# Optimization experiments

Measured on AMD Instinct MI355X. Metric: run time of the kernel, lower is better.

The kernel has to match this reference:

```python
import jax, jax.numpy as jnp
import numpy as np

NUM_TAGS = 5

def setup_inputs() -> dict:
    key = jax.random.key(0)
    ks = jax.random.split(key, 8)
    B, N, K, Q = 2, 5, 5, 4
    Ls, Lq, D = 128, 128, 768
    inp = {
        'support_token_embedding': jax.random.normal(ks[0], (B * N * K, Ls, D), jnp.float32),
        'query_token_embedding': jax.random.normal(ks[1], (B * N * Q, Lq, D), jnp.float32),
        'support_mask': jnp.ones((B * N * K, Ls), jnp.float32),
        'query_mask': jnp.ones((B * N * Q, Lq), jnp.float32),
        'support_entity_label': jax.random.normal(ks[2], (B * N * K, Ls, NUM_TAGS), jnp.float32),
        'proj_w': jax.random.normal(ks[3], (D, 4 * D), jnp.float32) * 0.02,
        'proj_b': jnp.zeros((D,), jnp.float32),
        'rel_w1': jax.random.normal(ks[4], (D, 4 * D), jnp.float32) * 0.02,
        'rel_b1': jnp.zeros((D,), jnp.float32),
        'rel_w2': jax.random.normal(ks[5], (1, D), jnp.float32) * 0.02,
        'rel_b2': jnp.zeros((1,), jnp.float32),
        'B': B, 'N': N, 'K': K, 'Q': Q,
    }
    return inp

def _fuse(m1, m2):
    return jnp.concatenate([m1, m2, jnp.abs(m1 - m2), m1 * m2], axis=-1)

def reference(support_token_embedding, query_token_embedding, support_mask, query_mask,
              support_entity_label, proj_w, proj_b, rel_w1, rel_b1, rel_w2, rel_b2,
              B, N, K, Q):
    D = support_token_embedding.shape[-1]
    Lq = query_token_embedding.shape[1]

    # ---- cal_bio: per-(sample,shot) tag prototypes, vectorized ----
    labels = jnp.argmax(support_entity_label, axis=-1)                 # [BNK, Ls]
    onehot = jax.nn.one_hot(labels, NUM_TAGS, dtype=jnp.float32)       # [BNK, Ls, T]
    # tag 0 ('O') is additionally gated by the support mask
    masks = jnp.concatenate([onehot[:, :, :1] * support_mask[:, :, None], onehot[:, :, 1:]], axis=2)
    sums = jnp.einsum('blt,bld->btd', masks, support_token_embedding)  # [BNK, T, D]
    cnt = jnp.sum(masks, axis=1)[:, :, None]                           # [BNK, T, 1]
    proto = jnp.where(cnt > 0, sums / jnp.maximum(cnt, 1.0), 0.0)      # [BNK, T, D]
    proto = proto.reshape(B * N, K, NUM_TAGS, D).mean(axis=1)          # mean over K shots
    proto = proto.reshape(B, N, NUM_TAGS, D)                           # support_BIO

    # ---- expand to all (query, class) pairs: batch = B*N*Q*N ----
    BQ = B * N * Q * N
    support = jnp.broadcast_to(proto[:, None], (B, N * Q, N, NUM_TAGS, D)).reshape(BQ, NUM_TAGS, D)
    query = jnp.broadcast_to(query_token_embedding.reshape(B, N * Q, 1, Lq, D),
                             (B, N * Q, N, Lq, D)).reshape(BQ, Lq, D)
    qmask = jnp.broadcast_to(query_mask.reshape(B, N * Q, 1, Lq),
                             (B, N * Q, N, Lq)).reshape(BQ, Lq, 1)
    smask = jnp.ones((BQ, NUM_TAGS, 1), jnp.float32)

    # ---- CoAttention with additive mask bias + post-softmax mask multiply ----
    att = jnp.einsum('bsd,bqd->bsq', support, query) + smask * jnp.swapaxes(qmask, 1, 2) * 100.0
    support_ = jnp.einsum('bsq,bqd->bsd', jax.nn.softmax(att, axis=2), query) * smask
    query_ = jnp.einsum('bqs,bsd->bqd', jax.nn.softmax(jnp.swapaxes(att, 1, 2), axis=2), support) * qmask

    # ---- fuse + proj + relu ----
    es = jax.nn.relu(_fuse(support, support_) @ proj_w.T + proj_b)     # [BQ, T, D]
    eq = jax.nn.relu(_fuse(query, query_) @ proj_w.T + proj_b)        # [BQ, Lq, D]

    # ---- local aggregation: masked max + mean pooling ----
    eq_agg = jnp.concatenate([jnp.max(eq, axis=1), jnp.sum(eq, axis=1) / jnp.sum(qmask, axis=1)], axis=1)
    es_agg = jnp.concatenate([jnp.max(es, axis=1), jnp.sum(es, axis=1) / jnp.sum(smask, axis=1)], axis=1)

    # ---- relation MLP ----
    cat_seq = jnp.concatenate([eq_agg, es_agg], axis=1)                # [BQ, 4D]
    h = jax.nn.relu(cat_seq @ rel_w1.T + rel_b1)
    logits = h @ rel_w2.T + rel_b2                                     # [BQ, 1]
    return logits.reshape(B * N * Q, N)
```

## Files before the change

### kernel.cpp

```cpp
#include <hip/hip_runtime.h>

typedef unsigned short u16;
typedef __attribute__((ext_vector_type(8))) short short8;
typedef __attribute__((ext_vector_type(4))) float f32x4;

#define B_   2
#define N_   5
#define K_   5
#define Q_   4
#define T_   5
#define D_   768
#define L_   128
#define BN_  (B_*N_)
#define BNK_ (B_*N_*K_)
#define BQ_  (B_*N_*Q_*N_)
#define K4_  (4*D_)
#define KFQ  1536
#define AROWS 144

#define QEMB_N  (40*128*768)
#define PROJW_N (768*3072)
#define R_PROTO1 5120
#define R_SUP    5248
#define R_PROTO2 6248
#define R_TOTAL  6400

__device__ __forceinline__ float bf2f(u16 u) {
    return __uint_as_float(((unsigned)u) << 16);
}
__device__ __forceinline__ u16 f2bf(float f) {
    unsigned u = __float_as_uint(f);
    return (u16)((u + 0x7fffu + ((u >> 16) & 1u)) >> 16);
}
__device__ __forceinline__ void gl_lds16(const u16* g, u16* l) {
    __builtin_amdgcn_global_load_lds(
        (const __attribute__((address_space(1))) unsigned int*)g,
        (__attribute__((address_space(3))) unsigned int*)l, 16, 0, 0);
}

__global__ void k_convert3(const float* __restrict__ q, const float* __restrict__ pw,
                           const float* __restrict__ rw, u16* __restrict__ qo,
                           u16* __restrict__ po, u16* __restrict__ ro) {
    const long n1 = QEMB_N / 4, n2 = PROJW_N / 4;
    const long total = n1 + 2 * n2;
    for (long i = (long)blockIdx.x * 256 + threadIdx.x; i < total; i += (long)gridDim.x * 256) {
        const float* src; u16* dst; long k;
        if (i < n1)            { src = q;  dst = qo; k = i; }
        else if (i < n1 + n2)  { src = pw; dst = po; k = i - n1; }
        else                   { src = rw; dst = ro; k = i - n1 - n2; }
        float4 v = ((const float4*)src)[k];
        u16 o[4] = {f2bf(v.x), f2bf(v.y), f2bf(v.z), f2bf(v.w)};
        *(uint2*)(dst + k * 4) = *(const uint2*)o;
    }
}

__global__ void k_proto_shot(const float* __restrict__ label, const float* __restrict__ smask,
                             const float* __restrict__ semb, float* __restrict__ proto_shot) {
    int bnk = blockIdx.x;
    int s = blockIdx.y;
    __shared__ int   s_tag[L_];
    __shared__ float s_w[L_];
    __shared__ float s_cnt[T_];
    int tid = threadIdx.x;
    if (tid < L_) {
        const float* lp = label + ((long)bnk * L_ + tid) * T_;
        float best = lp[0]; int bi = 0;
        #pragma unroll
        for (int t = 1; t < T_; ++t) { float v = lp[t]; if (v > best) { best = v; bi = t; } }
        s_tag[tid] = bi;
        s_w[tid]   = (bi == 0) ? smask[(long)bnk * L_ + tid] : 1.0f;
    }
    __syncthreads();
    if (tid < T_) {
        float c = 0.f;
        for (int l = 0; l < L_; ++l) if (s_tag[l] == tid) c += s_w[l];
        s_cnt[tid] = c;
    }
    __syncthreads();
    float acc[T_] = {};
    for (int l = 0; l < L_; ++l) {
        float w = s_w[l]; int tg = s_tag[l];
        float e = semb[((long)bnk * L_ + l) * D_ + tid + s * 256] * w;
        #pragma unroll
        for (int t = 0; t < T_; ++t) acc[t] += (tg == t) ? e : 0.0f;
    }
    int d = tid + s * 256;
    #pragma unroll
    for (int t = 0; t < T_; ++t) {
        float c = s_cnt[t];
        float v = (c > 0.f) ? acc[t] / fmaxf(c, 1.f) : 0.f;
        proto_shot[(bnk * T_ + t) * D_ + d] = v;
    }
}

__global__ void k_proto_mean(const float* __restrict__ proto_shot,
                             float* __restrict__ proto_f32, u16* __restrict__ A_all) {
    int bx = blockIdx.x;
    if (bx < 150) {
        int idx = bx * 256 + threadIdx.x;
        if (idx >= BN_ * T_ * D_) return;
        int r = idx / D_, d = idx - r * D_;
        int bn = r / T_;
        int rem = idx - bn * (T_ * D_);
        float s = 0.f;
        #pragma unroll
        for (int k = 0; k < K_; ++k) s += proto_shot[(bn * K_ + k) * (T_ * D_) + rem];
        s *= (1.f / K_);
        proto_f32[idx] = s;
        u16 b = f2bf(s);
        A_all[(size_t)(R_PROTO1 + r) * D_ + d] = b;
        A_all[(size_t)(R_PROTO2 + r) * D_ + d] = b;
    } else {
        int zidx = (bx - 150) * 256 + threadIdx.x;
        if (zidx >= 59904 + 78336) return;
        size_t off;
        if (zidx < 59904) off = (size_t)5170 * D_ + zidx;
        else              off = (size_t)6298 * D_ + (zidx - 59904);
        A_all[off] = 0;
    }
}

__global__ void k_attn(const float* __restrict__ qemb, const float* __restrict__ qmask_g,
                       const float* __restrict__ proto_f32,
                       u16* __restrict__ qf, u16* __restrict__ supA,
                       float* __restrict__ p2m_ws, float* __restrict__ qssum_ws) {
    int x = blockIdx.x;
    int xcd = x & 7, slot = x >> 3;
    int g = (slot / 5) * 8 + xcd;
    int n2 = slot % 5;
    int bq = g * 5 + n2;
    int q_idx = g;
    int bn = (bq / (N_ * Q_ * N_)) * N_ + (bq % N_);
    __shared__ float s_proto[T_ * D_];
    __shared__ float s_att[T_][L_];
    __shared__ float s_ps[T_][L_];
    __shared__ float s_qm[L_];
    int tid = threadIdx.x;
    for (int i = tid; i < T_ * D_; i += 256) s_proto[i] = proto_f32[bn * T_ * D_ + i];
    if (tid < L_) s_qm[tid] = qmask_g[(long)q_idx * L_ + tid];
    __syncthreads();
    for (int p = tid; p < T_ * L_; p += 256) {
        int t = p >> 7, q = p & (L_ - 1);
        const float* pp = s_proto + t * D_;
        const float4* qp = (const float4*)(qemb + ((size_t)q_idx * L_ + q) * D_);
        float acc = 0.f;
        #pragma unroll 4
        for (int d = 0; d < D_ / 4; ++d) {
            float4 v = qp[d];
            acc += v.x * pp[4 * d] + v.y * pp[4 * d + 1] + v.z * pp[4 * d + 2] + v.w * pp[4 * d + 3];
        }
        s_att[t][q] = acc + 100.f * s_qm[q];
    }
    __syncthreads();
    if (tid < T_) {
        int t = tid; float m = -1e30f;
        for (int q = 0; q < L_; ++q) m = fmaxf(m, s_att[t][q]);
        float ss = 0.f;
        for (int q = 0; q < L_; ++q) { float e = __expf(s_att[t][q] - m); s_ps[t][q] = e; ss += e; }
        float inv = 1.f / ss;
        for (int q = 0; q < L_; ++q) s_ps[t][q] *= inv;
    } else if (tid >= 128) {
        int q = tid - 128; float m = -1e30f;
        float e[T_];
        #pragma unroll
        for (int t = 0; t < T_; ++t) m = fmaxf(m, s_att[t][q]);
        float ss = 0.f;
        #pragma unroll
        for (int t = 0; t < T_; ++t) { e[t] = __expf(s_att[t][q] - m); ss += e[t]; }
        float inv = s_qm[q] / ss;
        #pragma unroll
        for (int t = 0; t < T_; ++t) p2m_ws[((size_t)bq * T_ + t) * L_ + q] = e[t] * inv;
    } else if (tid == 5) {
        float s = 0.f;
        for (int q = 0; q < L_; ++q) s += s_qm[q];
        qssum_ws[bq] = s;
    }
    __syncthreads();
    u16* qfb = qf + (size_t)bq * AROWS * KFQ;
    {
        float acc[T_][3] = {};
        #pragma unroll 4
        for (int q = 0; q < L_; ++q) {
            const float* qp = qemb + ((size_t)q_idx * L_ + q) * D_;
            float qv[3];
            #pragma unroll
            for (int s = 0; s < 3; ++s) qv[s] = qp[tid + s * 256];
            #pragma unroll
            for (int t = 0; t < T_; ++t) {
                float p = s_ps[t][q];
                #pragma unroll
                for (int s = 0; s < 3; ++s) acc[t][s] += p * qv[s];
            }
        }
        #pragma unroll
        for (int t = 0; t < T_; ++t) {
            u16* er = qfb + (size_t)(128 + t) * KFQ;
            #pragma unroll
            for (int s = 0; s < 3; ++s) {
                int d = tid + s * 256;
                float p = s_proto[t * D_ + d];
                float sv = acc[t][s];
                supA[((size_t)bq * T_ + t) * D_ + d] = f2bf(sv);
                er[d]       = f2bf(fabsf(p - sv));
                er[768 + d] = f2bf(p * sv);
            }
        }
    }
    {
        u16* pr2 = qfb + (size_t)133 * KFQ;
        short8 z = short8{0, 0, 0, 0, 0, 0, 0, 0};
        for (int i = tid; i < (11 * KFQ) / 8; i += 256) *(short8*)(pr2 + i * 8) = z;
    }
}

__global__ void k_qf(const float* __restrict__ qemb, const float* __restrict__ proto_f32,
                     const float* __restrict__ p2m, u16* __restrict__ qf) {
    int bq = blockIdx.x;
    int rg = blockIdx.y;
    int q_idx = bq / N_;
    int bn = (bq / (N_ * Q_ * N_)) * N_ + (bq % N_);
    __shared__ float s_proto[T_ * D_];
    __shared__ float s_p2[32][8];
    int tid = threadIdx.x;
    int w = tid >> 6, lane = tid & 63;
    for (int i = tid; i < T_ * D_; i += 256) s_proto[i] = proto_f32[bn * T_ * D_ + i];
    if (tid < 32 * T_) {
        int r = tid / T_, t = tid - r * T_;
        s_p2[r][t] = p2m[((size_t)bq * T_ + t) * L_ + rg * 32 + r];
    }
    __syncthreads();
    u16* qfb = qf + (size_t)bq * AROWS * KFQ;
    #pragma unroll
    for (int rr = 0; rr < 8; ++rr) {
        int rloc = w * 8 + rr;
        int row = rg * 32 + rloc;
        float p0 = s_p2[rloc][0], p1 = s_p2[rloc][1], p2v = s_p2[rloc][2];
        float p3 = s_p2[rloc][3], p4 = s_p2[rloc][4];
        const float* qrow = qemb + ((size_t)q_idx * L_ + row) * D_;
        u16* qr = qfb + (size_t)row * KFQ;
        #pragma unroll
        for (int ch = 0; ch < 12; ++ch) {
            int c = ch * 64 + lane;
            float m2 = p0 * s_proto[c] + p1 * s_proto[D_ + c] + p2v * s_proto[2 * D_ + c]
                     + p3 * s_proto[3 * D_ + c] + p4 * s_proto[4 * D_ + c];
            float qv = qrow[c];
            qr[c]       = f2bf(fabsf(qv - m2));
            qr[768 + c] = f2bf(qv * m2);
        }
    }
}

#define SUBGW ((128 + 128) * 32)
__global__ __launch_bounds__(256) void k_gemm_gw(const u16* __restrict__ A_all,
                                                 const u16* __restrict__ projw_bf,
                                                 u16* __restrict__ g1, u16* __restrict__ sw2,
                                                 u16* __restrict__ pw2) {
    int mbase = blockIdx.y * 128;
    int jbase = blockIdx.x * 128;
    int boff = (mbase >= R_SUP) ? 768 : 0;
    __shared__ __align__(16) u16 sT[2][2 * SUBGW];
    int tid = threadIdx.x;
    int lane = tid & 63, w = tid >> 6, quad = lane >> 4, l16 = lane & 15;
    int srow = lane >> 2, sko = lane & 3;
    const u16* Ab = A_all + ((size_t)mbase + srow) * D_ + sko * 8;
    const u16* Bb = projw_bf + (size_t)(jbase + srow) * K4_ + boff + sko * 8;

    f32x4 zero = {0.f, 0.f, 0.f, 0.f};
    f32x4 acc[8][2];
    #pragma unroll
    for (int rt = 0; rt < 8; ++rt) { acc[rt][0] = zero; acc[rt][1] = zero; }

    auto issue = [&](int kt, int b) {
        #pragma unroll
        for (int s = 0; s < 2; ++s) {
            int k0 = kt * 64 + s * 32;
            u16* base = sT[b] + s * SUBGW;
            gl_lds16(Ab + (size_t)(w * 16) * D_ + k0, base + (w * 16) * 32);
            gl_lds16(Ab + (size_t)(64 + w * 16) * D_ + k0, base + (64 + w * 16) * 32);
            gl_lds16(Bb + (size_t)(w * 16) * K4_ + k0, base + (128 + w * 16) * 32);
            gl_lds16(Bb + (size_t)(64 + w * 16) * K4_ + k0, base + (128 + 64 + w * 16) * 32);
        }
    };

    issue(0, 0);
    for (int kt = 0; kt < D_ / 64; ++kt) {
        int cur = kt & 1;
        __syncthreads();
        if (kt + 1 < D_ / 64) issue(kt + 1, 1 - cur);
        #pragma unroll
        for (int s = 0; s < 2; ++s) {
            const u16* base = sT[cur] + s * SUBGW;
            short8 bfr[2];
            #pragma unroll
            for (int jj = 0; jj < 2; ++jj)
                bfr[jj] = *(const short8*)(base + (128 + (w * 2 + jj) * 16 + l16) * 32 + quad * 8);
            #pragma unroll
            for (int rt = 0; rt < 8; ++rt) {
                short8 a = *(const short8*)(base + (rt * 16 + l16) * 32 + quad * 8);
                acc[rt][0] = __builtin_amdgcn_mfma_f32_16x16x32_bf16(a, bfr[0], acc[rt][0], 0, 0, 0);
                acc[rt][1] = __builtin_amdgcn_mfma_f32_16x16x32_bf16(a, bfr[1], acc[rt][1], 0, 0, 0);
            }
        }
    }
    #pragma unroll
    for (int jj = 0; jj < 2; ++jj) {
        int col = jbase + (w * 2 + jj) * 16 + l16;
        #pragma unroll
        for (int rt = 0; rt < 8; ++rt)
            #pragma unroll
            for (int r = 0; r < 4; ++r) {
                int row = mbase + rt * 16 + quad * 4 + r;
                u16 v = f2bf(acc[rt][jj][r]);
                if (row < R_SUP)            g1[(size_t)row * D_ + col] = v;
                else if (row < R_PROTO2)    sw2[(size_t)(row - R_SUP) * D_ + col] = v;
                else if (row < R_PROTO2+50) pw2[(size_t)(row - R_PROTO2) * D_ + col] = v;
            }
    }
}

#define SUBSZ ((AROWS + 128) * 32)
__global__ __launch_bounds__(256) void k_gemm_q(
        const u16* __restrict__ qf, const u16* __restrict__ projw_bf,
        const float* __restrict__ projb, const u16* __restrict__ g1,
        const u16* __restrict__ pw2, const u16* __restrict__ sw2,
        const float* __restrict__ p2m, const float* __restrict__ qssum_ws,
        u16* __restrict__ cat_ws) {
    int x = blockIdx.x;
    int xcd = x & 7, slot = x >> 3;
    int i = slot / 6, jslot = slot % 6;
    int g = (i / 5) * 8 + xcd;
    int bq = g * 5 + (i % 5);
    int jbase = jslot * 128;
    int q_idx = bq / N_;
    int bn = (bq / (N_ * Q_ * N_)) * N_ + (bq % N_);
    __shared__ __align__(16) u16 sT[2][2 * SUBSZ];
    __shared__ float s_p2mL[T_ * 128];
    __shared__ float s_pw2L[T_ * 128];
    int tid = threadIdx.x;
    int lane = tid & 63, w = tid >> 6, quad = lane >> 4, l16 = lane & 15;
    int srow = lane >> 2, sko = lane & 3;
    const u16* Ab = qf + ((size_t)bq * AROWS + srow) * KFQ + sko * 8;
    const u16* Bb = projw_bf + (size_t)(jbase + srow) * K4_ + 1536 + sko * 8;

    f32x4 zero = {0.f, 0.f, 0.f, 0.f};
    f32x4 acc[9][2];
    #pragma unroll
    for (int rt = 0; rt < 9; ++rt) { acc[rt][0] = zero; acc[rt][1] = zero; }

    auto issue = [&](int kt, int b) {
        #pragma unroll
        for (int s = 0; s < 2; ++s) {
            int k0 = kt * 64 + s * 32;
            u16* base = sT[b] + s * SUBSZ;
            gl_lds16(Ab + (size_t)(w * 16) * KFQ + k0, base + (w * 16) * 32);
            gl_lds16(Ab + (size_t)(64 + w * 16) * KFQ + k0, base + (64 + w * 16) * 32);
            if (w == 0) gl_lds16(Ab + (size_t)128 * KFQ + k0, base + 128 * 32);
            gl_lds16(Bb + (size_t)(w * 16) * K4_ + k0, base + (AROWS + w * 16) * 32);
            gl_lds16(Bb + (size_t)(64 + w * 16) * K4_ + k0, base + (AROWS + 64 + w * 16) * 32);
        }
    };

    issue(0, 0);
    for (int kt = 0; kt < KFQ / 64; ++kt) {
        int cur = kt & 1;
        __syncthreads();
        if (kt + 1 < KFQ / 64) issue(kt + 1, 1 - cur);
        #pragma unroll
        for (int s = 0; s < 2; ++s) {
            const u16* base = sT[cur] + s * SUBSZ;
            short8 bfr[2];
            #pragma unroll
            for (int jj = 0; jj < 2; ++jj)
                bfr[jj] = *(const short8*)(base + (AROWS + (w * 2 + jj) * 16 + l16) * 32 + quad * 8);
            #pragma unroll
            for (int rt = 0; rt < 9; ++rt) {
                short8 a = *(const short8*)(base + (rt * 16 + l16) * 32 + quad * 8);
                acc[rt][0] = __builtin_amdgcn_mfma_f32_16x16x32_bf16(a, bfr[0], acc[rt][0], 0, 0, 0);
                acc[rt][1] = __builtin_amdgcn_mfma_f32_16x16x32_bf16(a, bfr[1], acc[rt][1], 0, 0, 0);
            }
        }
    }
    for (int i2 = tid; i2 < T_ * 128; i2 += 256) {
        s_p2mL[i2] = p2m[(size_t)bq * (T_ * 128) + i2];
        s_pw2L[i2] = bf2f(pw2[(size_t)(bn * T_ + (i2 >> 7)) * D_ + jbase + (i2 & 127)]);
    }
    __syncthreads();
    float inv_qs = 1.f / qssum_ws[bq];
    #pragma unroll
    for (int jj = 0; jj < 2; ++jj) {
        int col = jbase + (w * 2 + jj) * 16 + l16;
        int cj = (w * 2 + jj) * 16 + l16;
        float bias = projb[col];
        float qmax = 0.f, qsum = 0.f, smax = 0.f, ssum = 0.f;
        #pragma unroll
        for (int rt = 0; rt < 8; ++rt) {
            #pragma unroll
            for (int r = 0; r < 4; ++r) {
                int row = rt * 16 + quad * 4 + r;
                float g1v = bf2f(g1[(size_t)(q_idx * 128 + row) * D_ + col]);
                float mix = s_p2mL[row] * s_pw2L[cj]
                          + s_p2mL[128 + row] * s_pw2L[128 + cj]
                          + s_p2mL[256 + row] * s_pw2L[256 + cj]
                          + s_p2mL[384 + row] * s_pw2L[384 + cj]
                          + s_p2mL[512 + row] * s_pw2L[512 + cj];
                float v = fmaxf(acc[rt][jj][r] + g1v + mix + bias, 0.f);
                qmax = fmaxf(qmax, v); qsum += v;
            }
        }
        #pragma unroll
        for (int r = 0; r < 4; ++r) {
            int t = quad * 4 + r;
            if (t < T_) {
                float g1v = bf2f(g1[(size_t)(5120 + bn * T_ + t) * D_ + col]);
                float s2v = bf2f(sw2[(size_t)(bq * T_ + t) * D_ + col]);
                float v = fmaxf(acc[8][jj][r] + g1v + s2v + bias, 0.f);
                smax = fmaxf(smax, v); ssum += v;
            }
        }
        qmax = fmaxf(qmax, __shfl_xor(qmax, 16, 64)); qmax = fmaxf(qmax, __shfl_xor(qmax, 32, 64));
        qsum += __shfl_xor(qsum, 16, 64);             qsum += __shfl_xor(qsum, 32, 64);
        smax = fmaxf(smax, __shfl_xor(smax, 16, 64)); smax = fmaxf(smax, __shfl_xor(smax, 32, 64));
        ssum += __shfl_xor(ssum, 16, 64);             ssum += __shfl_xor(ssum, 32, 64);
        if (quad == 0) {
            u16* cp = cat_ws + (size_t)bq * K4_;
            cp[col]           = f2bf(qmax);
            cp[D_ + col]      = f2bf(qsum * inv_qs);
            cp[2 * D_ + col]  = f2bf(smax);
            cp[3 * D_ + col]  = f2bf(ssum * 0.2f);
        }
    }
}

#define SUBRM ((64 + 128) * 32)
__global__ __launch_bounds__(256) void k_relmlp(const u16* __restrict__ cat_ws,
                                                const u16* __restrict__ w1,
                                                float* __restrict__ part) {
    int mbase = blockIdx.y * 64;
    int jbase = blockIdx.x * 128;
    int ks = blockIdx.z;
    __shared__ __align__(16) u16 sT[2][2 * SUBRM];
    int tid = threadIdx.x;
    int lane = tid & 63, w = tid >> 6, quad = lane >> 4, l16 = lane & 15;
    int srow = lane >> 2, sko = lane & 3;
    const u16* Ab = cat_ws + (size_t)(mbase + srow) * K4_ + ks * 384 + sko * 8;
    const u16* Bb = w1 + (size_t)(jbase + srow) * K4_ + ks * 384 + sko * 8;

    f32x4 zero = {0.f, 0.f, 0.f, 0.f};
    f32x4 acc[4][2];
    #pragma unroll
    for (int rt = 0; rt < 4; ++rt) { acc[rt][0] = zero; acc[rt][1] = zero; }

    auto issue = [&](int kt, int b) {
        #pragma unroll
        for (int s = 0; s < 2; ++s) {
            int k0 = kt * 64 + s * 32;
            u16* base = sT[b] + s * SUBRM;
            gl_lds16(Ab + (size_t)(w * 16) * K4_ + k0, base + (w * 16) * 32);
            gl_lds16(Bb + (size_t)(w * 16) * K4_ + k0, base + (64 + w * 16) * 32);
            gl_lds16(Bb + (size_t)(64 + w * 16) * K4_ + k0, base + (64 + 64 + w * 16) * 32);
        }
    };

    issue(0, 0);
    for (int kt = 0; kt < 6; ++kt) {
        int cur = kt & 1;
        __syncthreads();
        if (kt + 1 < 6) issue(kt + 1, 1 - cur);
        #pragma unroll
        for (int s = 0; s < 2; ++s) {
            const u16* base = sT[cur] + s * SUBRM;
            short8 bfr[2];
            #pragma unroll
            for (int jj = 0; jj < 2; ++jj)
                bfr[jj] = *(const short8*)(base + (64 + (2 * w + jj) * 16 + l16) * 32 + quad * 8);
            #pragma unroll
            for (int rt = 0; rt < 4; ++rt) {
                short8 a = *(const short8*)(base + (rt * 16 + l16) * 32 + quad * 8);
                acc[rt][0] = __builtin_amdgcn_mfma_f32_16x16x32_bf16(a, bfr[0], acc[rt][0], 0, 0, 0);
                acc[rt][1] = __builtin_amdgcn_mfma_f32_16x16x32_bf16(a, bfr[1], acc[rt][1], 0, 0, 0);
            }
        }
    }
    #pragma unroll
    for (int jj = 0; jj < 2; ++jj) {
        int col = jbase + (2 * w + jj) * 16 + l16;
        #pragma unroll
        for (int rt = 0; rt < 4; ++rt) {
            #pragma unroll
            for (int r = 0; r < 4; ++r) {
                int grow = mbase + rt * 16 + quad * 4 + r;
                if (grow < BQ_)
                    part[((size_t)ks * BQ_ + grow) * D_ + col] = acc[rt][jj][r];
            }
        }
    }
}

__global__ void k_rel_fin(const float* __restrict__ part, const float* __restrict__ b1,
                          const float* __restrict__ w2, const float* __restrict__ b2,
                          float* __restrict__ out) {
    int bq = blockIdx.x, tid = threadIdx.x;
    float a = 0.f;
    #pragma unroll
    for (int s = 0; s < 3; ++s) {
        int col = tid + s * 256;
        float sum = 0.f;
        #pragma unroll
        for (int ks = 0; ks < 8; ++ks) sum += part[((size_t)ks * BQ_ + bq) * D_ + col];
        float h = fmaxf(sum + b1[col], 0.f);
        a += h * w2[col];
    }
    __shared__ float red[256];
    red[tid] = a; __syncthreads();
    for (int off = 128; off >= 1; off >>= 1) {
        if (tid < off) red[tid] += red[tid + off];
        __syncthreads();
    }
    if (tid == 0) out[bq] = red[0] + b2[0];
}

extern "C" void kernel_launch(void* const* d_in, const int* in_sizes, int n_in,
                              void* d_out, int out_size, void* d_ws, size_t ws_size,
                              hipStream_t stream) {
    (void)in_sizes; (void)n_in; (void)out_size; (void)ws_size;
    const float* semb  = (const float*)d_in[0];
    const float* qemb  = (const float*)d_in[1];
    const float* smask = (const float*)d_in[2];
    const float* qmask = (const float*)d_in[3];
    const float* label = (const float*)d_in[4];
    const float* projw = (const float*)d_in[5];
    const float* projb = (const float*)d_in[6];
    const float* relw1 = (const float*)d_in[7];
    const float* relb1 = (const float*)d_in[8];
    const float* relw2 = (const float*)d_in[9];
    const float* relb2 = (const float*)d_in[10];

    char* ws = (char*)d_ws;
    u16*   A_all     = (u16*)  (ws + 0);
    u16*   projw_bf  = (u16*)  (ws + 9830400);
    u16*   relw1_bf  = (u16*)  (ws + 14548992);
    float* proto_shot= (float*)(ws + 19267584);
    float* proto_f32 = (float*)(ws + 20035584);
    float* qssum     = (float*)(ws + 20189184);
    float* p2m_ws    = (float*)(ws + 20190080);
    u16*   pw2_ws    = (u16*)  (ws + 20702080);
    u16*   sw2_ws    = (u16*)  (ws + 20778880);
    u16*   cat_ws    = (u16*)  (ws + 22314880);
    u16*   g1_ws     = (u16*)  (ws + 23543680);
    float* part_ws   = (float*)(ws + 31604608);
    u16*   qf_ws     = (u16*)  (ws + 36519808);

    k_convert3<<<2048, 256, 0, stream>>>(qemb, projw, relw1, A_all, projw_bf, relw1_bf);
    k_proto_shot<<<dim3(BNK_, 3), 256, 0, stream>>>(label, smask, semb, proto_shot);
    k_proto_mean<<<691, 256, 0, stream>>>(proto_shot, proto_f32, A_all);
    k_attn<<<BQ_, 256, 0, stream>>>(qemb, qmask, proto_f32, qf_ws, A_all + (size_t)R_SUP * D_,
                                    p2m_ws, qssum);
    k_qf<<<dim3(BQ_, 4), 256, 0, stream>>>(qemb, proto_f32, p2m_ws, qf_ws);
    k_gemm_gw<<<dim3(6, 50), 256, 0, stream>>>(A_all, projw_bf, g1_ws, sw2_ws, pw2_ws);
    k_gemm_q<<<1200, 256, 0, stream>>>(qf_ws, projw_bf, projb, g1_ws, pw2_ws, sw2_ws,
                                       p2m_ws, qssum, cat_ws);
    k_relmlp<<<dim3(6, 4, 8), 256, 0, stream>>>(cat_ws, relw1_bf, part_ws);
    k_rel_fin<<<BQ_, 256, 0, stream>>>(part_ws, relb1, relw2, relb2, (float*)d_out);
}
```

Measured before the change: 483.5 us.

## Pre-tile GEMM operands into MFMA fragment layout and load directly to registers

```diff
diff --git a/kernel.cpp b/kernel.cpp
--- a/kernel.cpp
+++ b/kernel.cpp
@@ -17,13 +17,13 @@
 #define K4_  (4*D_)
 #define KFQ  1536
 #define AROWS 144
+#define NKT  48
 
 #define QEMB_N  (40*128*768)
 #define PROJW_N (768*3072)
 #define R_PROTO1 5120
 #define R_SUP    5248
 #define R_PROTO2 6248
-#define R_TOTAL  6400
 
 __device__ __forceinline__ float bf2f(u16 u) {
     return __uint_as_float(((unsigned)u) << 16);
@@ -54,6 +54,19 @@
     }
 }
 
+__global__ void k_tileB(const float* __restrict__ pw, u16* __restrict__ pwt) {
+    int tidx = blockIdx.x * 4 + (threadIdx.x >> 6);
+    int lane = threadIdx.x & 63, n = lane & 15, quad = lane >> 4;
+    int jt = tidx / NKT, kt = tidx - jt * NKT;
+    const float* src = pw + (size_t)(jt * 16 + n) * K4_ + 1536 + kt * 32 + quad * 8;
+    float4 v0 = *(const float4*)src, v1 = *(const float4*)(src + 4);
+    float qv[8] = {v0.x, v0.y, v0.z, v0.w, v1.x, v1.y, v1.z, v1.w};
+    short8 o;
+    #pragma unroll
+    for (int i = 0; i < 8; ++i) o[i] = (short)f2bf(qv[i]);
+    *(short8*)(pwt + (size_t)tidx * 512 + n * 32 + quad * 8) = o;
+}
+
 __global__ void k_proto_shot(const float* __restrict__ label, const float* __restrict__ smask,
                              const float* __restrict__ semb, float* __restrict__ proto_shot) {
     int bnk = blockIdx.x;
@@ -122,7 +135,7 @@
 
 __global__ void k_attn(const float* __restrict__ qemb, const float* __restrict__ qmask_g,
                        const float* __restrict__ proto_f32,
-                       u16* __restrict__ qf, u16* __restrict__ supA,
+                       u16* __restrict__ qft, u16* __restrict__ supA,
                        float* __restrict__ p2m_ws, float* __restrict__ qssum_ws) {
     int x = blockIdx.x;
     int xcd = x & 7, slot = x >> 3;
@@ -176,7 +189,7 @@
         qssum_ws[bq] = s;
     }
     __syncthreads();
-    u16* qfb = qf + (size_t)bq * AROWS * KFQ;
+    u16* et = qft + ((size_t)(bq * 9 + 8) * NKT) * 512;
     {
         float acc[T_][3] = {};
         #pragma unroll 4
@@ -194,59 +207,62 @@
         }
         #pragma unroll
         for (int t = 0; t < T_; ++t) {
-            u16* er = qfb + (size_t)(128 + t) * KFQ;
             #pragma unroll
             for (int s = 0; s < 3; ++s) {
                 int d = tid + s * 256;
                 float p = s_proto[t * D_ + d];
                 float sv = acc[t][s];
                 supA[((size_t)bq * T_ + t) * D_ + d] = f2bf(sv);
-                er[d]       = f2bf(fabsf(p - sv));
-                er[768 + d] = f2bf(p * sv);
+                int kt = d >> 5, c = d & 31;
+                et[(size_t)kt * 512 + t * 32 + c]        = f2bf(fabsf(p - sv));
+                et[(size_t)(24 + kt) * 512 + t * 32 + c] = f2bf(p * sv);
             }
         }
     }
     {
-        u16* pr2 = qfb + (size_t)133 * KFQ;
-        short8 z = short8{0, 0, 0, 0, 0, 0, 0, 0};
-        for (int i = tid; i < (11 * KFQ) / 8; i += 256) *(short8*)(pr2 + i * 8) = z;
+        for (int i = tid; i < NKT * 11 * 32; i += 256) {
+            int kt = i / 352, rem = i - kt * 352;
+            int r = 5 + (rem >> 5), c = rem & 31;
+            et[(size_t)kt * 512 + r * 32 + c] = 0;
+        }
     }
 }
 
 __global__ void k_qf(const float* __restrict__ qemb, const float* __restrict__ proto_f32,
-                     const float* __restrict__ p2m, u16* __restrict__ qf) {
+                     const float* __restrict__ p2m, u16* __restrict__ qft) {
     int bq = blockIdx.x;
-    int rg = blockIdx.y;
+    int rt = blockIdx.y;
     int q_idx = bq / N_;
     int bn = (bq / (N_ * Q_ * N_)) * N_ + (bq % N_);
     __shared__ float s_proto[T_ * D_];
-    __shared__ float s_p2[32][8];
+    __shared__ float s_p2[16][8];
     int tid = threadIdx.x;
-    int w = tid >> 6, lane = tid & 63;
+    int w = tid >> 6, lane = tid & 63, r = lane & 15, quad = lane >> 4;
     for (int i = tid; i < T_ * D_; i += 256) s_proto[i] = proto_f32[bn * T_ * D_ + i];
-    if (tid < 32 * T_) {
-        int r = tid / T_, t = tid - r * T_;
-        s_p2[r][t] = p2m[((size_t)bq * T_ + t) * L_ + rg * 32 + r];
-    }
-    __syncthreads();
-    u16* qfb = qf + (size_t)bq * AROWS * KFQ;
-    #pragma unroll
-    for (int rr = 0; rr < 8; ++rr) {
-        int rloc = w * 8 + rr;
-        int row = rg * 32 + rloc;
-        float p0 = s_p2[rloc][0], p1 = s_p2[rloc][1], p2v = s_p2[rloc][2];
-        float p3 = s_p2[rloc][3], p4 = s_p2[rloc][4];
-        const float* qrow = qemb + ((size_t)q_idx * L_ + row) * D_;
-        u16* qr = qfb + (size_t)row * KFQ;
-        #pragma unroll
-        for (int ch = 0; ch < 12; ++ch) {
-            int c = ch * 64 + lane;
-            float m2 = p0 * s_proto[c] + p1 * s_proto[D_ + c] + p2v * s_proto[2 * D_ + c]
-                     + p3 * s_proto[3 * D_ + c] + p4 * s_proto[4 * D_ + c];
-            float qv = qrow[c];
-            qr[c]       = f2bf(fabsf(qv - m2));
-            qr[768 + c] = f2bf(qv * m2);
-        }
+    if (tid < 16 * T_) {
+        int rr = tid / T_, t = tid - rr * T_;
+        s_p2[rr][t] = p2m[((size_t)bq * T_ + t) * L_ + rt * 16 + rr];
+    }
+    __syncthreads();
+    int row = rt * 16 + r;
+    float p0 = s_p2[r][0], p1 = s_p2[r][1], p2v = s_p2[r][2], p3 = s_p2[r][3], p4 = s_p2[r][4];
+    const float* qrow = qemb + ((size_t)q_idx * L_ + row) * D_;
+    u16* qtb = qft + ((size_t)(bq * 9 + rt) * NKT) * 512 + r * 32 + quad * 8;
+    for (int kt = w; kt < NKT; kt += 4) {
+        int dbase = ((kt < 24) ? kt : kt - 24) * 32 + quad * 8;
+        float4 v0 = *(const float4*)(qrow + dbase);
+        float4 v1 = *(const float4*)(qrow + dbase + 4);
+        float qv[8] = {v0.x, v0.y, v0.z, v0.w, v1.x, v1.y, v1.z, v1.w};
+        short8 o;
+        #pragma unroll
+        for (int i = 0; i < 8; ++i) {
+            int d = dbase + i;
+            float m2 = p0 * s_proto[d] + p1 * s_proto[D_ + d] + p2v * s_proto[2 * D_ + d]
+                     + p3 * s_proto[3 * D_ + d] + p4 * s_proto[4 * D_ + d];
+            float v = (kt < 24) ? fabsf(qv[i] - m2) : qv[i] * m2;
+            o[i] = (short)f2bf(v);
+        }
+        *(short8*)(qtb + (size_t)kt * 512) = o;
     }
 }
 
@@ -318,9 +334,8 @@
     }
 }
 
-#define SUBSZ ((AROWS + 128) * 32)
 __global__ __launch_bounds__(256) void k_gemm_q(
-        const u16* __restrict__ qf, const u16* __restrict__ projw_bf,
+        const u16* __restrict__ qft, const u16* __restrict__ pwt,
         const float* __restrict__ projb, const u16* __restrict__ g1,
         const u16* __restrict__ pw2, const u16* __restrict__ sw2,
         const float* __restrict__ p2m, const float* __restrict__ qssum_ws,
@@ -333,52 +348,43 @@
     int jbase = jslot * 128;
     int q_idx = bq / N_;
     int bn = (bq / (N_ * Q_ * N_)) * N_ + (bq % N_);
-    __shared__ __align__(16) u16 sT[2][2 * SUBSZ];
     __shared__ float s_p2mL[T_ * 128];
     __shared__ float s_pw2L[T_ * 128];
     int tid = threadIdx.x;
     int lane = tid & 63, w = tid >> 6, quad = lane >> 4, l16 = lane & 15;
-    int srow = lane >> 2, sko = lane & 3;
-    const u16* Ab = qf + ((size_t)bq * AROWS + srow) * KFQ + sko * 8;
-    const u16* Bb = projw_bf + (size_t)(jbase + srow) * K4_ + 1536 + sko * 8;
+    int loff = l16 * 32 + quad * 8;
+
+    const u16* Ab = qft + (size_t)bq * 9 * NKT * 512 + loff;
+    const u16* Bb = pwt + (size_t)(jslot * 8 + w * 2) * NKT * 512 + loff;
 
     f32x4 zero = {0.f, 0.f, 0.f, 0.f};
     f32x4 acc[9][2];
     #pragma unroll
     for (int rt = 0; rt < 9; ++rt) { acc[rt][0] = zero; acc[rt][1] = zero; }
 
-    auto issue = [&](int kt, int b) {
-        #pragma unroll
-        for (int s = 0; s < 2; ++s) {
-            int k0 = kt * 64 + s * 32;
-            u16* base = sT[b] + s * SUBSZ;
-            gl_lds16(Ab + (size_t)(w * 16) * KFQ + k0, base + (w * 16) * 32);
-            gl_lds16(Ab + (size_t)(64 + w * 16) * KFQ + k0, base + (64 + w * 16) * 32);
-            if (w == 0) gl_lds16(Ab + (size_t)128 * KFQ + k0, base + 128 * 32);
-            gl_lds16(Bb + (size_t)(w * 16) * K4_ + k0, base + (AROWS + w * 16) * 32);
-            gl_lds16(Bb + (size_t)(64 + w * 16) * K4_ + k0, base + (AROWS + 64 + w * 16) * 32);
-        }
+    short8 a0[9], b0[2], a1[9], b1[2];
+    auto loadf = [&](short8* A, short8* Bf, int kt) {
+        #pragma unroll
+        for (int rt = 0; rt < 9; ++rt)
+            A[rt] = *(const short8*)(Ab + (size_t)(rt * NKT + kt) * 512);
+        #pragma unroll
+        for (int jj = 0; jj < 2; ++jj)
+            Bf[jj] = *(const short8*)(Bb + (size_t)(jj * NKT + kt) * 512);
     };
-
-    issue(0, 0);
-    for (int kt = 0; kt < KFQ / 64; ++kt) {
-        int cur = kt & 1;
-        __syncthreads();
-        if (kt + 1 < KFQ / 64) issue(kt + 1, 1 - cur);
-        #pragma unroll
-        for (int s = 0; s < 2; ++s) {
-            const u16* base = sT[cur] + s * SUBSZ;
-            short8 bfr[2];
-            #pragma unroll
-            for (int jj = 0; jj < 2; ++jj)
-                bfr[jj] = *(const short8*)(base + (AROWS + (w * 2 + jj) * 16 + l16) * 32 + quad * 8);
-            #pragma unroll
-            for (int rt = 0; rt < 9; ++rt) {
-                short8 a = *(const short8*)(base + (rt * 16 + l16) * 32 + quad * 8);
-                acc[rt][0] = __builtin_amdgcn_mfma_f32_16x16x32_bf16(a, bfr[0], acc[rt][0], 0, 0, 0);
-                acc[rt][1] = __builtin_amdgcn_mfma_f32_16x16x32_bf16(a, bfr[1], acc[rt][1], 0, 0, 0);
-            }
-        }
+    auto domfma = [&](short8* A, short8* Bf) {
+        #pragma unroll
+        for (int rt = 0; rt < 9; ++rt) {
+            acc[rt][0] = __builtin_amdgcn_mfma_f32_16x16x32_bf16(A[rt], Bf[0], acc[rt][0], 0, 0, 0);
+            acc[rt][1] = __builtin_amdgcn_mfma_f32_16x16x32_bf16(A[rt], Bf[1], acc[rt][1], 0, 0, 0);
+        }
+    };
+
+    loadf(a0, b0, 0);
+    for (int kt = 0; kt < NKT; kt += 2) {
+        loadf(a1, b1, kt + 1);
+        domfma(a0, b0);
+        if (kt + 2 < NKT) loadf(a0, b0, kt + 2);
+        domfma(a1, b1);
     }
     for (int i2 = tid; i2 < T_ * 128; i2 += 256) {
         s_p2mL[i2] = p2m[(size_t)bq * (T_ * 128) + i2];
@@ -548,16 +554,18 @@
     u16*   cat_ws    = (u16*)  (ws + 22314880);
     u16*   g1_ws     = (u16*)  (ws + 23543680);
     float* part_ws   = (float*)(ws + 31604608);
-    u16*   qf_ws     = (u16*)  (ws + 36519808);
+    u16*   pwt_ws    = (u16*)  (ws + 36519808);
+    u16*   qft_ws    = (u16*)  (ws + 38879104);
 
     k_convert3<<<2048, 256, 0, stream>>>(qemb, projw, relw1, A_all, projw_bf, relw1_bf);
+    k_tileB<<<576, 256, 0, stream>>>(projw, pwt_ws);
     k_proto_shot<<<dim3(BNK_, 3), 256, 0, stream>>>(label, smask, semb, proto_shot);
     k_proto_mean<<<691, 256, 0, stream>>>(proto_shot, proto_f32, A_all);
-    k_attn<<<BQ_, 256, 0, stream>>>(qemb, qmask, proto_f32, qf_ws, A_all + (size_t)R_SUP * D_,
+    k_attn<<<BQ_, 256, 0, stream>>>(qemb, qmask, proto_f32, qft_ws, A_all + (size_t)R_SUP * D_,
                                     p2m_ws, qssum);
-    k_qf<<<dim3(BQ_, 4), 256, 0, stream>>>(qemb, proto_f32, p2m_ws, qf_ws);
+    k_qf<<<dim3(BQ_, 8), 256, 0, stream>>>(qemb, proto_f32, p2m_ws, qft_ws);
     k_gemm_gw<<<dim3(6, 50), 256, 0, stream>>>(A_all, projw_bf, g1_ws, sw2_ws, pw2_ws);
-    k_gemm_q<<<1200, 256, 0, stream>>>(qf_ws, projw_bf, projb, g1_ws, pw2_ws, sw2_ws,
+    k_gemm_q<<<1200, 256, 0, stream>>>(qft_ws, pwt_ws, projb, g1_ws, pw2_ws, sw2_ws,
                                        p2m_ws, qssum, cat_ws);
     k_relmlp<<<dim3(6, 4, 8), 256, 0, stream>>>(cat_ws, relw1_bf, part_ws);
     k_rel_fin<<<BQ_, 256, 0, stream>>>(part_ws, relb1, relw2, relb2, (float*)d_out);
```

After: 483.0 us. About the same (-0.1%).
